# Kernel optimization log

Hardware: AMD Instinct MI355X
Metric: run time of the kernel (lower is better)

The kernel has to match this reference:

```python
import math
import jax, jax.numpy as jnp
import numpy as np

B, C, E = 8, 2048, 1024

def setup_inputs() -> dict:
    key = jax.random.key(0)
    ks = jax.random.split(key, 7)
    s_e = 1.0 / math.sqrt(E)
    s_c = 1.0 / math.sqrt(C)
    return {
        'x': jax.random.normal(ks[0], (B, C, E), dtype=jnp.float32),
        'fc_w': jax.random.normal(ks[1], (E, E), dtype=jnp.float32) * s_e,
        'fc_b': jax.random.normal(ks[2], (E,), dtype=jnp.float32) * s_e,
        'alt_fc_w': jax.random.normal(ks[3], (C, C), dtype=jnp.float32) * s_c,
        'alt_fc_b': jax.random.normal(ks[4], (C,), dtype=jnp.float32) * s_c,
        'vfc_w': jax.random.normal(ks[5], (E, E), dtype=jnp.float32) * s_e,
        'vfc_b': jax.random.normal(ks[6], (E,), dtype=jnp.float32) * s_e,
    }

def reference(x, fc_w, fc_b, alt_fc_w, alt_fc_b, vfc_w, vfc_b):
    # y = fc(x): [b,c,e]
    y = jnp.einsum('bce,fe->bcf', x, fc_w) + fc_b
    # yx = alt_fc(x^T): [b,e,c] -> Linear over context dim -> [b,e,k]
    xx = jnp.swapaxes(x, 1, 2)                    # [b,e,c]
    yx = jnp.einsum('bec,kc->bek', xx, alt_fc_w) + alt_fc_b
    # attention scores: [b,c,k]
    attn = jnp.einsum('bce,bek->bck', y, yx)
    scale = 1.0 / math.sqrt(attn.shape[-1])
    attn = jax.nn.softmax(attn * scale, axis=-1)
    # values
    vx = jnp.einsum('bke,fe->bkf', x, vfc_w) + vfc_b
    out = jnp.einsum('bck,bke->bce', attn, vx)
    # post_feed=None -> return y only
    return out
```

## Files before the change

### kernel.cpp

```cpp
#include <hip/hip_runtime.h>
#include <stdint.h>

#define Bb 8
#define Cc 2048
#define Ee 1024

typedef unsigned short u16;
typedef __attribute__((ext_vector_type(8))) short short8;
typedef __attribute__((ext_vector_type(4))) float f32x4;

__device__ __forceinline__ u16 f2bf(float f){
    unsigned u = __builtin_bit_cast(unsigned, f);
    return (u16)((u + 0x7fffu + ((u >> 16) & 1u)) >> 16);
}
__device__ __forceinline__ void gld16(const void* g, void* l){
    __builtin_amdgcn_global_load_lds(
        (const __attribute__((address_space(1))) unsigned int*)g,
        (__attribute__((address_space(3))) unsigned int*)l,
        16, 0, 0);
}
#define MFMA(a,b,c) __builtin_amdgcn_mfma_f32_16x16x32_bf16((a),(b),(c),0,0,0)
#define SBAR()  __builtin_amdgcn_s_barrier()
#define SCHED0() __builtin_amdgcn_sched_barrier(0)
#define LGKM8() asm volatile("s_waitcnt lgkmcnt(8)" ::: "memory")
#define LGKM4() asm volatile("s_waitcnt lgkmcnt(4)" ::: "memory")
#define LGKM0() asm volatile("s_waitcnt lgkmcnt(0)" ::: "memory")
#define VMCNT0() asm volatile("s_waitcnt vmcnt(0)" ::: "memory")

struct Seg {
    const u16* A; const u16* Bm; void* C; const float* bias; float* extra;
    int N, K, gx, gy;
    long sA, sB, sC;
    float scale;
    int bias_mode;
    int epi;
    int out_f32;
};
struct Desc { Seg s0, s1, s2; int n0, n1; };

__global__ __launch_bounds__(256) void k_prep(const float* __restrict__ x,
                                              u16* __restrict__ xb, u16* __restrict__ xbT,
                                              const float* __restrict__ fw, u16* __restrict__ fwb,
                                              const float* __restrict__ vw, u16* __restrict__ vwb,
                                              const float* __restrict__ aw, u16* __restrict__ awb){
    __shared__ float tile[32][33];
    const int blk = blockIdx.x;
    if (blk < 16384){
        const int cx = blk & 31;
        const int rest = blk >> 5;
        const int cy = rest & 63;
        const int b  = rest >> 6;
        const float* src = x + (long)b * Cc * Ee;
        u16* xbp  = xb  + (long)b * Cc * Ee;
        u16* xbTp = xbT + (long)b * Cc * Ee;
        const int c0 = cx * 32;
        const int r0 = cy * 32;
        const int tx = threadIdx.x & 31;
        const int ty = threadIdx.x >> 5;
        #pragma unroll
        for (int p = 0; p < 4; ++p){
            float v = src[(long)(r0 + ty + p*8) * Ee + c0 + tx];
            tile[ty + p*8][tx] = v;
            xbp[(long)(r0 + ty + p*8) * Ee + c0 + tx] = f2bf(v);
        }
        __syncthreads();
        #pragma unroll
        for (int p = 0; p < 4; ++p)
            xbTp[(long)(c0 + ty + p*8) * Cc + r0 + tx] = f2bf(tile[tx][ty + p*8]);
    } else {
        const long n0 = (long)Ee * Ee / 4, n1 = n0, n2 = (long)Cc * Cc / 4;
        long i = (long)(blk - 16384) * 256 + threadIdx.x;
        const long stride = 2048L * 256;
        const long tot = n0 + n1 + n2;
        for (; i < tot; i += stride){
            const float* s; u16* d; long k;
            if (i < n0)          { s = fw; d = fwb; k = i; }
            else if (i < n0 + n1){ s = vw; d = vwb; k = i - n0; }
            else                 { s = aw; d = awb; k = i - n0 - n1; }
            float4 f = ((const float4*)s)[k];
            ((ushort4*)d)[k] = make_ushort4(f2bf(f.x), f2bf(f.y), f2bf(f.z), f2bf(f.w));
        }
    }
}

__global__ __launch_bounds__(512, 2)
void k_gemm_multi(Desc d)
{
    __shared__ __attribute__((aligned(16))) char smem[131072];

    const int blk = (int)blockIdx.x;
    Seg S; int lin;
    if (blk < d.n0)            { S = d.s0; lin = blk; }
    else if (blk < d.n0 + d.n1){ S = d.s1; lin = blk - d.n0; }
    else                       { S = d.s2; lin = blk - d.n0 - d.n1; }

    const int nwg = S.gx * S.gy * Bb;
    const int swz = (lin & 7) * (nwg >> 3) + (lin >> 3);
    const int bx = swz % S.gx;
    const int tmp = swz / S.gx;
    const int by = tmp % S.gy;
    const int bz = tmp / S.gy;

    const u16* A  = S.A  + (long)bz * S.sA;
    const u16* Bm = S.Bm + (long)bz * S.sB;
    const int  N = S.N, K = S.K;
    u16*   Cm = (u16*)S.C + (long)bz * S.sC;
    float* Cf = (float*)S.C + (long)bz * S.sC;

    const int tid  = threadIdx.x;
    const int lane = tid & 63;
    const int wave = tid >> 6;
    const int wr = wave >> 2;
    const int wc = wave & 3;
    const int tileM = bx * 256;
    const int tileN = by * 256;

    const int srow   = tid >> 3;
    const int schunk = (tid & 7) ^ (srow & 7);
    const u16* Ag = A  + (long)(tileM + srow) * K + schunk * 8;
    const u16* Bg = Bm + (long)(tileN + srow) * K + schunk * 8;
    const long uK = (long)64 * K;
    const int  ldst = tid * 16;

    const int lrow = lane & 15;
    const int lk   = lane >> 4;
    const int sw   = lrow & 7;
    const int cs0  = ((0 + lk) ^ sw) * 16;
    const int cs1  = ((4 + lk) ^ sw) * 16;
    const int arow0 = (wr*128 + lrow) * 128;
    const int brow0 = 32768 + (wc*64 + lrow) * 128;

    f32x4 acc[8][4];
    #pragma unroll
    for (int m = 0; m < 8; ++m)
        #pragma unroll
        for (int n = 0; n < 4; ++n)
            acc[m][n] = (f32x4){0.f,0.f,0.f,0.f};

    char* sm = smem;
    #pragma unroll
    for (int u = 0; u < 4; ++u) gld16(Bg + u*uK, sm + 32768 + u*8192 + ldst);
    #pragma unroll
    for (int u = 0; u < 4; ++u) gld16(Ag + u*uK, sm + u*8192 + ldst);
    __syncthreads();

    const int NT = K >> 6;
    short8 aE[4], aO[4], bE[4], bO[4];

    for (int t = 0; t < NT; ++t){
        const bool pref = (t + 1) < NT;
        char* cbuf = sm + ((t & 1) << 16);
        char* nbuf = sm + (((t + 1) & 1) << 16);
        const u16* Agt = Ag + (long)(t + 1) * 64;
        const u16* Bgt = Bg + (long)(t + 1) * 64;

        if (pref){
            gld16(Agt + 0*uK, nbuf + 0*8192 + ldst);
            gld16(Agt + 1*uK, nbuf + 1*8192 + ldst);
            gld16(Agt + 2*uK, nbuf + 2*8192 + ldst);
            gld16(Agt + 3*uK, nbuf + 3*8192 + ldst);
            gld16(Bgt + 0*uK, nbuf + 32768 + 0*8192 + ldst);
            gld16(Bgt + 1*uK, nbuf + 32768 + 1*8192 + ldst);
            gld16(Bgt + 2*uK, nbuf + 32768 + 2*8192 + ldst);
            gld16(Bgt + 3*uK, nbuf + 32768 + 3*8192 + ldst);
        }

        #pragma unroll
        for (int m = 0; m < 4; ++m) aE[m] = *(const short8*)(cbuf + arow0 + m*2048 + cs0);
        #pragma unroll
        for (int n = 0; n < 4; ++n) bE[n] = *(const short8*)(cbuf + brow0 + n*2048 + cs0);
        #pragma unroll
        for (int m = 0; m < 4; ++m) aO[m] = *(const short8*)(cbuf + arow0 + (m+4)*2048 + cs0);

        LGKM4(); SCHED0();
        #pragma unroll
        for (int m = 0; m < 4; ++m)
            #pragma unroll
            for (int n = 0; n < 4; ++n)
                acc[m][n] = MFMA(aE[m], bE[n], acc[m][n]);

        #pragma unroll
        for (int m = 0; m < 4; ++m) aE[m] = *(const short8*)(cbuf + arow0 + m*2048 + cs1);
        #pragma unroll
        for (int n = 0; n < 4; ++n) bO[n] = *(const short8*)(cbuf + brow0 + n*2048 + cs1);
        LGKM8(); SCHED0();
        #pragma unroll
        for (int m = 0; m < 4; ++m)
            #pragma unroll
            for (int n = 0; n < 4; ++n)
                acc[m+4][n] = MFMA(aO[m], bE[n], acc[m+4][n]);

        #pragma unroll
        for (int m = 0; m < 4; ++m) aO[m] = *(const short8*)(cbuf + arow0 + (m+4)*2048 + cs1);
        LGKM4(); SCHED0();
        #pragma unroll
        for (int m = 0; m < 4; ++m)
            #pragma unroll
            for (int n = 0; n < 4; ++n)
                acc[m][n] = MFMA(aE[m], bO[n], acc[m][n]);

        LGKM0(); SCHED0();
        #pragma unroll
        for (int m = 0; m < 4; ++m)
            #pragma unroll
            for (int n = 0; n < 4; ++n)
                acc[m+4][n] = MFMA(aO[m], bO[n], acc[m+4][n]);

        VMCNT0(); SBAR(); SCHED0();
    }

    const int r0base = tileM + wr*128 + lk*4;
    const int cbase  = tileN + wc*64 + lrow;

    if (S.epi == 0){
        const float scale = S.scale;
        #pragma unroll
        for (int m = 0; m < 8; ++m){
            const int r0 = r0base + m*16;
            #pragma unroll
            for (int n = 0; n < 4; ++n){
                const int c = cbase + n*16;
                f32x4 v = acc[m][n];
                #pragma unroll
                for (int j = 0; j < 4; ++j){
                    float val = v[j] * scale;
                    if (S.bias_mode == 1) val += S.bias[c];
                    if (S.bias_mode == 2) val += S.bias[r0 + j];
                    if (S.out_f32) Cf[(long)(r0 + j) * N + c] = val;
                    else           Cm[(long)(r0 + j) * N + c] = f2bf(val);
                }
            }
        }
    } else if (S.epi == 1){
        const float scale = S.scale;
        float* lsum = (float*)smem;
        const int rl0 = wr*128 + lk*4;
        #pragma unroll
        for (int m = 0; m < 8; ++m){
            const int r0 = r0base + m*16;
            #pragma unroll
            for (int j = 0; j < 4; ++j){
                float rp = 0.f;
                #pragma unroll
                for (int n = 0; n < 4; ++n){
                    float e = __expf(acc[m][n][j] * scale);
                    rp += e;
                    Cm[(long)(r0 + j) * N + (cbase + n*16)] = f2bf(e);
                }
                rp += __shfl_xor(rp, 1);
                rp += __shfl_xor(rp, 2);
                rp += __shfl_xor(rp, 4);
                rp += __shfl_xor(rp, 8);
                if (lrow == 0)
                    lsum[(rl0 + m*16 + j)*4 + wc] = rp;
            }
        }
        __syncthreads();
        if (tid < 256){
            float4 v4 = ((const float4*)lsum)[tid];
            S.extra[((long)bz*Cc + tileM + tid)*8 + by] = v4.x + v4.y + v4.z + v4.w;
        }
    } else {
        #pragma unroll
        for (int m = 0; m < 8; ++m){
            const int r0 = r0base + m*16;
            #pragma unroll
            for (int j = 0; j < 4; ++j){
                const float4* pr = (const float4*)(S.extra + ((long)bz*Cc + r0 + j)*8);
                float4 pa = pr[0], pb = pr[1];
                float Ssum = pa.x+pa.y+pa.z+pa.w + pb.x+pb.y+pb.z+pb.w;
                const float inv = 1.f / Ssum;
                #pragma unroll
                for (int n = 0; n < 4; ++n)
                    Cf[(long)(r0 + j) * N + (cbase + n*16)] = acc[m][n][j] * inv;
            }
        }
    }
}

extern "C" void kernel_launch(void* const* d_in, const int* in_sizes, int n_in,
                              void* d_out, int out_size, void* d_ws, size_t ws_size,
                              hipStream_t stream)
{
    const float* x     = (const float*)d_in[0];
    const float* fc_w  = (const float*)d_in[1];
    const float* fc_b  = (const float*)d_in[2];
    const float* altw  = (const float*)d_in[3];
    const float* altb  = (const float*)d_in[4];
    const float* vfc_w = (const float*)d_in[5];
    const float* vfc_b = (const float*)d_in[6];
    float* out = (float*)d_out;

    char* ws = (char*)d_ws;
    const size_t nBCE = (size_t)Bb * Cc * Ee;
    u16* xb   = (u16*)(ws);
    u16* xbT  = (u16*)(ws + 2 * nBCE);
    u16* P    = (u16*)(ws);
    u16* y    = (u16*)(ws + 4 * nBCE);
    u16* z    = (u16*)(ws + 6 * nBCE);
    u16* vxT  = (u16*)(ws + 8 * nBCE);
    u16* fcwb = (u16*)(ws + 10 * nBCE);
    u16* vfwb = fcwb + (size_t)Ee * Ee;
    u16* awb  = vfwb + (size_t)Ee * Ee;
    float* rpart = (float*)(ws + 10 * nBCE + 2*((size_t)Ee*Ee*2 + (size_t)Cc*Cc));

    const long sBCE = (long)Cc * Ee;
    const long sBCC = (long)Cc * Cc;

    k_prep<<<18432, 256, 0, stream>>>(x, xb, xbT, fc_w, fcwb, vfc_w, vfwb, altw, awb);

    Desc d1;
    d1.s0 = Seg{ awb, xbT, z, altb, nullptr, Ee, Cc, 8, 4, 0, sBCE, sBCE, 1.f, 2, 0, 0 };
    d1.s1 = Seg{ xb, fcwb, y, fc_b, nullptr, Ee, Ee, 8, 4, sBCE, 0, sBCE, 1.f, 1, 0, 0 };
    d1.s2 = Seg{ vfwb, xb, vxT, vfc_b, nullptr, Cc, Ee, 4, 8, 0, sBCE, sBCE, 1.f, 2, 0, 0 };
    d1.n0 = 256; d1.n1 = 256;
    k_gemm_multi<<<768, 512, 0, stream>>>(d1);

    Desc d2;
    d2.s0 = Seg{ y, z, P, nullptr, rpart, Cc, Ee, 8, 8, sBCE, sBCE, sBCC, 0.022097086912079608f, 0, 1, 0 };
    d2.s1 = d2.s0; d2.s2 = d2.s0;
    d2.n0 = 512; d2.n1 = 0;
    k_gemm_multi<<<512, 512, 0, stream>>>(d2);

    Desc d3;
    d3.s0 = Seg{ P, vxT, out, nullptr, rpart, Ee, Cc, 8, 4, sBCC, sBCE, sBCE, 1.f, 0, 2, 1 };
    d3.s1 = d3.s0; d3.s2 = d3.s0;
    d3.n0 = 256; d3.n1 = 0;
    k_gemm_multi<<<256, 512, 0, stream>>>(d3);
}
```

Before: 353.7 us.

## Template GEMM kernel and fuse fc/vfc projections into one concatenated-weight GEMM

Replaces the runtime segment-descriptor GEMM with a kernel templated on bias mode, output type and epilogue, so the per-element branches on those flags are resolved at compile time. The fc and vfc projections now run as a single GEMM with N=2048, on the assumption that the two bf16 weight matrices sit next to each other in the workspace. A new epilogue writes the first half to y with the fc bias and the second half transposed into vxT with the vfc bias, using vector stores. The single multi-segment launch becomes two separate launches, which adds a kernel boundary but lets each GEMM use its own grid.

After: 300.9 us. -14.9%, faster.

```diff
diff --git a/kernel.cpp b/kernel.cpp
--- a/kernel.cpp
+++ b/kernel.cpp
@@ -26,17 +26,6 @@
 #define LGKM4() asm volatile("s_waitcnt lgkmcnt(4)" ::: "memory")
 #define LGKM0() asm volatile("s_waitcnt lgkmcnt(0)" ::: "memory")
 #define VMCNT0() asm volatile("s_waitcnt vmcnt(0)" ::: "memory")
-
-struct Seg {
-    const u16* A; const u16* Bm; void* C; const float* bias; float* extra;
-    int N, K, gx, gy;
-    long sA, sB, sC;
-    float scale;
-    int bias_mode;
-    int epi;
-    int out_f32;
-};
-struct Desc { Seg s0, s1, s2; int n0, n1; };
 
 __global__ __launch_bounds__(256) void k_prep(const float* __restrict__ x,
                                               u16* __restrict__ xb, u16* __restrict__ xbT,
@@ -83,29 +72,28 @@
     }
 }
 
+template<int BIAS_MODE, int OUT_F32, int EPI>
 __global__ __launch_bounds__(512, 2)
-void k_gemm_multi(Desc d)
+void k_gemm256(const u16* __restrict__ A, const u16* __restrict__ Bm,
+               void* __restrict__ Cout, const float* __restrict__ bias,
+               const float* __restrict__ bias2, float* __restrict__ extra,
+               int N, int K, long sA, long sB, long sC, float scale)
 {
     __shared__ __attribute__((aligned(16))) char smem[131072];
 
-    const int blk = (int)blockIdx.x;
-    Seg S; int lin;
-    if (blk < d.n0)            { S = d.s0; lin = blk; }
-    else if (blk < d.n0 + d.n1){ S = d.s1; lin = blk - d.n0; }
-    else                       { S = d.s2; lin = blk - d.n0 - d.n1; }
-
-    const int nwg = S.gx * S.gy * Bb;
+    const int gx = gridDim.x, gy = gridDim.y;
+    const int nwg = gx * gy * gridDim.z;
+    const int lin = blockIdx.x + gx * (blockIdx.y + gy * blockIdx.z);
     const int swz = (lin & 7) * (nwg >> 3) + (lin >> 3);
-    const int bx = swz % S.gx;
-    const int tmp = swz / S.gx;
-    const int by = tmp % S.gy;
-    const int bz = tmp / S.gy;
-
-    const u16* A  = S.A  + (long)bz * S.sA;
-    const u16* Bm = S.Bm + (long)bz * S.sB;
-    const int  N = S.N, K = S.K;
-    u16*   Cm = (u16*)S.C + (long)bz * S.sC;
-    float* Cf = (float*)S.C + (long)bz * S.sC;
+    const int bx = swz % gx;
+    const int tmp = swz / gx;
+    const int by = tmp % gy;
+    const int bz = tmp / gy;
+
+    const u16* Ap  = A  + (long)bz * sA;
+    const u16* Bp  = Bm + (long)bz * sB;
+    u16*   Cm = (u16*)Cout + (long)bz * sC;
+    float* Cf = (float*)Cout + (long)bz * sC;
 
     const int tid  = threadIdx.x;
     const int lane = tid & 63;
@@ -117,8 +105,8 @@
 
     const int srow   = tid >> 3;
     const int schunk = (tid & 7) ^ (srow & 7);
-    const u16* Ag = A  + (long)(tileM + srow) * K + schunk * 8;
-    const u16* Bg = Bm + (long)(tileN + srow) * K + schunk * 8;
+    const u16* Ag = Ap + (long)(tileM + srow) * K + schunk * 8;
+    const u16* Bg = Bp + (long)(tileN + srow) * K + schunk * 8;
     const long uK = (long)64 * K;
     const int  ldst = tid * 16;
 
@@ -212,8 +200,7 @@
     const int r0base = tileM + wr*128 + lk*4;
     const int cbase  = tileN + wc*64 + lrow;
 
-    if (S.epi == 0){
-        const float scale = S.scale;
+    if (EPI == 0){
         #pragma unroll
         for (int m = 0; m < 8; ++m){
             const int r0 = r0base + m*16;
@@ -224,15 +211,14 @@
                 #pragma unroll
                 for (int j = 0; j < 4; ++j){
                     float val = v[j] * scale;
-                    if (S.bias_mode == 1) val += S.bias[c];
-                    if (S.bias_mode == 2) val += S.bias[r0 + j];
-                    if (S.out_f32) Cf[(long)(r0 + j) * N + c] = val;
-                    else           Cm[(long)(r0 + j) * N + c] = f2bf(val);
+                    if (BIAS_MODE == 1) val += bias[c];
+                    if (BIAS_MODE == 2) val += bias[r0 + j];
+                    if (OUT_F32) Cf[(long)(r0 + j) * N + c] = val;
+                    else         Cm[(long)(r0 + j) * N + c] = f2bf(val);
                 }
             }
         }
-    } else if (S.epi == 1){
-        const float scale = S.scale;
+    } else if (EPI == 1){
         float* lsum = (float*)smem;
         const int rl0 = wr*128 + lk*4;
         #pragma unroll
@@ -258,21 +244,51 @@
         __syncthreads();
         if (tid < 256){
             float4 v4 = ((const float4*)lsum)[tid];
-            S.extra[((long)bz*Cc + tileM + tid)*8 + by] = v4.x + v4.y + v4.z + v4.w;
-        }
-    } else {
+            extra[((long)bz*Cc + tileM + tid)*8 + by] = v4.x + v4.y + v4.z + v4.w;
+        }
+    } else if (EPI == 2){
         #pragma unroll
         for (int m = 0; m < 8; ++m){
             const int r0 = r0base + m*16;
             #pragma unroll
             for (int j = 0; j < 4; ++j){
-                const float4* pr = (const float4*)(S.extra + ((long)bz*Cc + r0 + j)*8);
+                const float4* pr = (const float4*)(extra + ((long)bz*Cc + r0 + j)*8);
                 float4 pa = pr[0], pb = pr[1];
                 float Ssum = pa.x+pa.y+pa.z+pa.w + pb.x+pb.y+pb.z+pb.w;
                 const float inv = 1.f / Ssum;
                 #pragma unroll
                 for (int n = 0; n < 4; ++n)
                     Cf[(long)(r0 + j) * N + (cbase + n*16)] = acc[m][n][j] * inv;
+            }
+        }
+    } else {
+        if (tileN < 1024){
+            #pragma unroll
+            for (int m = 0; m < 8; ++m){
+                const int r0 = r0base + m*16;
+                #pragma unroll
+                for (int n = 0; n < 4; ++n){
+                    const int c = cbase + n*16;
+                    f32x4 v = acc[m][n];
+                    #pragma unroll
+                    for (int j = 0; j < 4; ++j)
+                        Cm[(long)(r0 + j) * Ee + c] = f2bf(v[j] + bias[c]);
+                }
+            }
+        } else {
+            u16* vxp = (u16*)extra + (long)bz * sC;
+            #pragma unroll
+            for (int m = 0; m < 8; ++m){
+                const int r0 = r0base + m*16;
+                #pragma unroll
+                for (int n = 0; n < 4; ++n){
+                    const int c = cbase + n*16;
+                    const float b2 = bias2[c - 1024];
+                    f32x4 v = acc[m][n];
+                    ushort4 o = make_ushort4(f2bf(v[0]+b2), f2bf(v[1]+b2),
+                                             f2bf(v[2]+b2), f2bf(v[3]+b2));
+                    *(ushort4*)&vxp[(long)(c - 1024) * Cc + r0] = o;
+                }
             }
         }
     }
@@ -306,25 +322,19 @@
 
     const long sBCE = (long)Cc * Ee;
     const long sBCC = (long)Cc * Cc;
+    dim3 blk(512);
 
     k_prep<<<18432, 256, 0, stream>>>(x, xb, xbT, fc_w, fcwb, vfc_w, vfwb, altw, awb);
 
-    Desc d1;
-    d1.s0 = Seg{ awb, xbT, z, altb, nullptr, Ee, Cc, 8, 4, 0, sBCE, sBCE, 1.f, 2, 0, 0 };
-    d1.s1 = Seg{ xb, fcwb, y, fc_b, nullptr, Ee, Ee, 8, 4, sBCE, 0, sBCE, 1.f, 1, 0, 0 };
-    d1.s2 = Seg{ vfwb, xb, vxT, vfc_b, nullptr, Cc, Ee, 4, 8, 0, sBCE, sBCE, 1.f, 2, 0, 0 };
-    d1.n0 = 256; d1.n1 = 256;
-    k_gemm_multi<<<768, 512, 0, stream>>>(d1);
-
-    Desc d2;
-    d2.s0 = Seg{ y, z, P, nullptr, rpart, Cc, Ee, 8, 8, sBCE, sBCE, sBCC, 0.022097086912079608f, 0, 1, 0 };
-    d2.s1 = d2.s0; d2.s2 = d2.s0;
-    d2.n0 = 512; d2.n1 = 0;
-    k_gemm_multi<<<512, 512, 0, stream>>>(d2);
-
-    Desc d3;
-    d3.s0 = Seg{ P, vxT, out, nullptr, rpart, Ee, Cc, 8, 4, sBCC, sBCE, sBCE, 1.f, 0, 2, 1 };
-    d3.s1 = d3.s0; d3.s2 = d3.s0;
-    d3.n0 = 256; d3.n1 = 0;
-    k_gemm_multi<<<256, 512, 0, stream>>>(d3);
-}
+    k_gemm256<2, 0, 0><<<dim3(8, 4, Bb), blk, 0, stream>>>(
+        awb, xbT, z, altb, nullptr, nullptr, Ee, Cc, 0, sBCE, sBCE, 1.f);
+
+    k_gemm256<0, 0, 3><<<dim3(8, 8, Bb), blk, 0, stream>>>(
+        xb, fcwb, y, fc_b, vfc_b, (float*)vxT, 2048, Ee, sBCE, 0, sBCE, 1.f);
+
+    k_gemm256<0, 0, 1><<<dim3(8, 8, Bb), blk, 0, stream>>>(
+        y, z, P, nullptr, nullptr, rpart, Cc, Ee, sBCE, sBCE, sBCC, 0.022097086912079608f);
+
+    k_gemm256<0, 1, 2><<<dim3(8, 4, Bb), blk, 0, stream>>>(
+        P, vxT, out, nullptr, nullptr, rpart, Ee, Cc, sBCC, sBCE, sBCE, 1.f);
+}
```
